# Optimization experiments

Measured on AMD Instinct MI355X. Metric: run time of the kernel, lower is better.

## Reference

```python
import jax, jax.numpy as jnp
import numpy as np

B, C, H, W = 16, 128, 128, 128
HEADS, DH = 4, 32          # hidden_dim = 128
GROUPS = 32                # min(dim // 4, 32)
EPS = 1e-5                 # eqx GroupNorm default


def setup_inputs() -> dict:
    key = jax.random.key(0)
    ks = jax.random.split(key, 8)
    hid = HEADS * DH
    return {
        "x": jax.random.normal(ks[0], (B, C, H, W), jnp.float32),
        "cond": jax.random.normal(ks[1], (B, C, H, W), jnp.float32),
        "gn_scale": jnp.ones((C,), jnp.float32),
        "gn_bias": jnp.zeros((C,), jnp.float32),
        "kv_w": jax.random.normal(ks[2], (2 * hid, C), jnp.float32) * 0.05,
        "kv_b": jax.random.normal(ks[3], (2 * hid,), jnp.float32) * 0.05,
        "q_w": jax.random.normal(ks[4], (hid, C), jnp.float32) * 0.05,
        "q_b": jax.random.normal(ks[5], (hid,), jnp.float32) * 0.05,
        "out_w": jax.random.normal(ks[6], (C, hid), jnp.float32) * 0.05,
        "out_b": jax.random.normal(ks[7], (C,), jnp.float32) * 0.05,
    }


def reference(x, cond, gn_scale, gn_bias, kv_w, kv_b, q_w, q_b, out_w, out_b):
    b, c, h, w = x.shape
    n = h * w
    # --- GroupNorm(32, dim) on x ---
    xg = x.reshape(b, GROUPS, c // GROUPS, h, w)
    mu = xg.mean(axis=(2, 3, 4), keepdims=True)
    var = xg.var(axis=(2, 3, 4), keepdims=True)
    xn = ((xg - mu) * jax.lax.rsqrt(var + EPS)).reshape(b, c, h, w)
    xn = xn * gn_scale[None, :, None, None] + gn_bias[None, :, None, None]
    # --- 1x1 conv projections (channel matmuls) ---
    kv = jnp.einsum('oc,bchw->bohw', kv_w, xn) + kv_b[None, :, None, None]
    q = jnp.einsum('oc,bchw->bohw', q_w, cond) + q_b[None, :, None, None]
    # split: channel layout is (kv, heads, dh)
    kv = kv.reshape(b, 2, HEADS, DH, n)
    k, v = kv[:, 0], kv[:, 1]          # [b, heads, dh, n]
    q = q.reshape(b, HEADS, DH, n)
    # --- linear-time attention: softmax over spatial positions ---
    k = jax.nn.softmax(k, axis=-1)
    context = jnp.einsum('bhdn,bhen->bhde', k, v)   # [b, heads, dh, dh]
    out = jnp.einsum('bhde,bhdn->bhen', context, q)  # [b, heads, dh, n]
    out = out.reshape(b, HEADS * DH, h, w)
    return jnp.einsum('oc,bchw->bohw', out_w, out) + out_b[None, :, None, None]
```

## Files before the change

### kernel.cpp

```cpp
#include <hip/hip_runtime.h>
#include <hip/hip_bf16.h>
#include <cstddef>

#define BATCH 16
#define CC 128
#define NN 16384
#define GROUPS 32
#define EPSV 1e-5f

#define OFF_MU    0
#define OFF_RSTD  512
#define OFF_BEFF  1024
#define OFF_CTX   5120
#define OFF_CB    70656
#define OFF_WH    334848
#define OFF_AH    596992
#define OFF_AL    728064
#define OFF_PART  859136
#define OFF_XT    5184512
#define PART_STRIDE 4224

typedef __attribute__((ext_vector_type(8))) short bf8;
typedef __attribute__((ext_vector_type(4))) float f4;
#define MFMA16(a,b,c) __builtin_amdgcn_mfma_f32_16x16x32_bf16(a,b,c,0,0,0)

__device__ inline unsigned short bf16_rtn(float f) {
    unsigned u = __builtin_bit_cast(unsigned, f);
    unsigned r = (u + 0x7FFFu + ((u >> 16) & 1u)) >> 16;
    return (unsigned short)r;
}
__device__ inline float bf16_f(unsigned short h) {
    unsigned u = ((unsigned)h) << 16;
    return __builtin_bit_cast(float, u);
}
__device__ inline unsigned cvtpk_bf16(float a, float b) {
    unsigned r;
    asm("v_cvt_pk_bf16_f32 %0, %1, %2" : "=v"(r) : "v"(a), "v"(b));
    return r;
}

__global__ __launch_bounds__(256) void k1a_fused(const float* __restrict__ src,
        unsigned short* __restrict__ xt, float* __restrict__ gp) {
    int b = blockIdx.y; int p0 = blockIdx.x * 128; int t = threadIdx.x;
    __shared__ unsigned short lh[128 * 136];
    int p = t & 127, chalf = t >> 7;
    const float* sp = src + (size_t)b * CC * NN + p0 + p;
    #pragma unroll 8
    for (int i = 0; i < 64; ++i) {
        int c = i * 2 + chalf;
        float v = sp[(size_t)c * NN];
        lh[p * 136 + c] = bf16_rtn(v);
    }
    __syncthreads();
    {
        int g = t >> 3, i8 = t & 7;
        float s = 0.f, sq = 0.f;
        for (int pp = i8 * 16; pp < i8 * 16 + 16; ++pp) {
            #pragma unroll
            for (int cc = 0; cc < 4; ++cc) {
                float v = bf16_f(lh[pp * 136 + g * 4 + cc]);
                s += v; sq += v * v;
            }
        }
        __shared__ float rs[256], rq[256];
        rs[t] = s; rq[t] = sq;
        __syncthreads();
        if (t < 32) {
            float a = 0.f, bq = 0.f;
            #pragma unroll
            for (int k = 0; k < 8; ++k) { a += rs[t * 8 + k]; bq += rq[t * 8 + k]; }
            float* d = gp + ((size_t)(b * 128 + blockIdx.x) * 32 + t) * 2;
            d[0] = a; d[1] = bq;
        }
    }
    int pr = t >> 4, c8 = (t & 15) * 8;
    #pragma unroll
    for (int j = 0; j < 8; ++j) {
        int p2 = j * 16 + pr;
        bf8 vh = *(const bf8*)&lh[p2 * 136 + c8];
        *(bf8*)&xt[((size_t)b * NN + p0 + p2) * 128 + c8] = vh;
    }
}

__global__ void k1b_stats(const float* __restrict__ gp, float* __restrict__ wsf) {
    int b = blockIdx.x; int t = threadIdx.x;
    int g = t & 31, sl = t >> 5;
    float s = 0.f, sq = 0.f;
    for (int j = sl; j < 128; j += 8) {
        const float* p = gp + ((size_t)(b * 128 + j) * 32 + g) * 2;
        s += p[0]; sq += p[1];
    }
    __shared__ float rs[256], rq[256];
    rs[t] = s; rq[t] = sq; __syncthreads();
    if (t < 32) {
        #pragma unroll
        for (int k = 1; k < 8; ++k) { s += rs[t + 32 * k]; sq += rq[t + 32 * k]; }
        float mean = s * (1.f / 65536.f);
        float var  = sq * (1.f / 65536.f) - mean * mean;
        wsf[OFF_MU + b * 32 + t]   = mean;
        wsf[OFF_RSTD + b * 32 + t] = rsqrtf(var + EPSV);
    }
}

__global__ __launch_bounds__(256) void k2_weff(const float* __restrict__ kv_w,
                        const float* __restrict__ kv_b,
                        const float* __restrict__ gn_scale, const float* __restrict__ gn_bias,
                        float* __restrict__ wsf, unsigned short* __restrict__ wh) {
    int b = blockIdx.y;
    int o0 = blockIdx.x * 32;
    int t = threadIdx.x;
    __shared__ float wrow[32 * 128];
    __shared__ float scl[128], sbm[128];
    __shared__ float bred[32][8];
    {
        const float4* src = (const float4*)(kv_w + (size_t)o0 * 128);
        float4* dst = (float4*)wrow;
        #pragma unroll
        for (int i = 0; i < 4; ++i) dst[i * 256 + t] = src[i * 256 + t];
        if (t < 128) {
            int g = t >> 2;
            float r = wsf[OFF_RSTD + b * 32 + g];
            float m = wsf[OFF_MU + b * 32 + g];
            float sc = gn_scale[t] * r;
            scl[t] = sc;
            sbm[t] = gn_bias[t] - m * sc;
        }
    }
    __syncthreads();
    int ol = t >> 3;
    int o  = o0 + ol;
    int q  = t & 7;
    {
        float bacc = 0.f;
        const float* wr = &wrow[ol * 128 + q * 16];
        #pragma unroll
        for (int c = 0; c < 16; ++c) bacc += wr[c] * sbm[q * 16 + c];
        bred[ol][q] = bacc;
    }
    int h  = (o & 127) >> 5;
    int ct = ((o >> 4) & 1) + ((o >= 128) ? 2 : 0);
    #pragma unroll
    for (int f2 = 0; f2 < 2; ++f2) {
        int f = 2 * q + f2;
        int ks = f >> 2, eq = f & 3;
        int c0 = ks * 32 + eq * 8;
        bf8 pk;
        #pragma unroll
        for (int e = 0; e < 8; ++e)
            pk[e] = (short)bf16_rtn(wrow[ol * 128 + c0 + e] * scl[c0 + e]);
        int lane = (o & 15) + 16 * eq;
        size_t fo = ((((size_t)b * 4 + h) * 4 + ct) * 4 + ks) * 512 + (size_t)lane * 8;
        *(bf8*)&wh[fo] = pk;
    }
    __syncthreads();
    if (q == 0) {
        float bacc = 0.f;
        #pragma unroll
        for (int k = 0; k < 8; ++k) bacc += bred[ol][k];
        wsf[OFF_BEFF + b * 256 + o] = kv_b[o] + bacc;
    }
}

__global__ __launch_bounds__(256) void k3_attn(
    const unsigned short* __restrict__ xt,
    const unsigned short* __restrict__ wh, const float* __restrict__ wsf,
    float* __restrict__ part)
{
    int b = blockIdx.y, chunk = blockIdx.x;
    int t = threadIdx.x, h = t >> 6, l = t & 63;
    int l15 = l & 15, lq = l >> 4;

    __shared__ unsigned short lds[4][2][32 * 64];

    bf8 W[4][4];
    #pragma unroll
    for (int ct = 0; ct < 4; ++ct)
      #pragma unroll
      for (int ks = 0; ks < 4; ++ks)
        W[ct][ks] = ((const bf8*)wh)[((((size_t)b*4 + h)*4 + ct)*4 + ks)*64 + l];

    float bk[4];
    #pragma unroll
    for (int ct = 0; ct < 4; ++ct) {
        int o = (ct < 2) ? (32*h + 16*ct + l15) : (128 + 32*h + 16*(ct-2) + l15);
        bk[ct] = wsf[OFF_BEFF + b * 256 + o];
    }

    bf8 ones;
    #pragma unroll
    for (int j = 0; j < 8; ++j) ones[j] = (short)0x3F80;

    f4 ctx[2][2]; f4 zac[2];
    #pragma unroll
    for (int i = 0; i < 2; ++i) {
        zac[i] = (f4){0,0,0,0};
        #pragma unroll
        for (int j = 0; j < 2; ++j) ctx[i][j] = (f4){0,0,0,0};
    }

    int pbase = chunk * 256;
    const unsigned short* xbase = xt + ((size_t)b * NN + pbase + l15) * 128 + lq * 8;
    #define FRAG(fp, ks) (*(const bf8*)(xbase + (size_t)(fp) * 2048 + (ks) * 32))

    bf8 pre[2][4];
    #pragma unroll
    for (int i = 0; i < 2; ++i)
      #pragma unroll
      for (int ks = 0; ks < 4; ++ks) pre[i][ks] = FRAG(i, ks);

    for (int tile = 0; tile < 4; ++tile) {
        #pragma unroll
        for (int half = 0; half < 2; ++half) {
            int nfp = tile * 4 + half * 2 + 2;
            int cfp = (nfp < 16) ? nfp : 0;
            bf8 nxt[2][4];
            #pragma unroll
            for (int i = 0; i < 2; ++i)
              #pragma unroll
              for (int ks = 0; ks < 4; ++ks) nxt[i][ks] = FRAG(cfp + i, ks);
            #pragma unroll
            for (int i = 0; i < 2; ++i) {
                int pt = half * 2 + i;
                f4 a4[4];
                #pragma unroll
                for (int ct = 0; ct < 4; ++ct) a4[ct] = (f4){0,0,0,0};
                #pragma unroll
                for (int ks = 0; ks < 4; ++ks) {
                    #pragma unroll
                    for (int ct = 0; ct < 4; ++ct)
                        a4[ct] = MFMA16(pre[i][ks], W[ct][ks], a4[ct]);
                }
                int p = pt * 16 + lq * 4;
                #pragma unroll
                for (int ct = 0; ct < 4; ++ct) {
                    int row = (ct & 1) * 16 + l15;
                    int sel = ct >> 1;
                    float v0 = a4[ct][0] + bk[ct];
                    float v1 = a4[ct][1] + bk[ct];
                    float v2 = a4[ct][2] + bk[ct];
                    float v3 = a4[ct][3] + bk[ct];
                    if (sel == 0) {
                        v0 = __expf(v0); v1 = __expf(v1);
                        v2 = __expf(v2); v3 = __expf(v3);
                    }
                    unsigned lo32 = cvtpk_bf16(v0, v1);
                    unsigned hi32 = cvtpk_bf16(v2, v3);
                    unsigned byte = ((unsigned)(row * 128 + p * 2)) ^ (((unsigned)(row & 7)) << 4);
                    *(uint2*)((char*)&lds[h][sel][0] + byte) = make_uint2(lo32, hi32);
                }
            }
            #pragma unroll
            for (int i = 0; i < 2; ++i)
              #pragma unroll
              for (int ks = 0; ks < 4; ++ks) pre[i][ks] = nxt[i][ks];
        }
        #pragma unroll
        for (int ks2 = 0; ks2 < 2; ++ks2) {
            int p8 = ks2 * 32 + lq * 8;
            bf8 ek[2], vv[2];
            #pragma unroll
            for (int dt = 0; dt < 2; ++dt) {
                int row = dt * 16 + l15;
                unsigned byte = ((unsigned)(row * 128 + p8 * 2)) ^ (((unsigned)(row & 7)) << 4);
                ek[dt] = *(const bf8*)((char*)&lds[h][0][0] + byte);
                vv[dt] = *(const bf8*)((char*)&lds[h][1][0] + byte);
            }
            #pragma unroll
            for (int dt = 0; dt < 2; ++dt) {
                #pragma unroll
                for (int et = 0; et < 2; ++et)
                    ctx[dt][et] = MFMA16(ek[dt], vv[et], ctx[dt][et]);
                zac[dt] = MFMA16(ek[dt], ones, zac[dt]);
            }
        }
    }
    #undef FRAG
    float* pb = part + (size_t)(b * 64 + chunk) * PART_STRIDE;
    #pragma unroll
    for (int dt = 0; dt < 2; ++dt) {
        #pragma unroll
        for (int et = 0; et < 2; ++et)
            #pragma unroll
            for (int j = 0; j < 4; ++j) {
                int d = 32*h + dt*16 + lq*4 + j;
                int e = et*16 + l15;
                pb[d * 32 + e] = ctx[dt][et][j];
            }
        if (l15 == 0)
            #pragma unroll
            for (int j = 0; j < 4; ++j)
                pb[4096 + 32*h + dt*16 + lq*4 + j] = zac[dt][j];
    }
}

__global__ __launch_bounds__(256) void k4_reduce(const float* __restrict__ part,
                                                 float* __restrict__ wsf, int nbpb) {
    int q = blockIdx.x, b = blockIdx.y;
    int tid = threadIdx.x;
    int hdl = tid >> 3;
    int hd = q * 32 + hdl;
    int e0 = (tid & 7) * 4;
    float s[4] = {0.f, 0.f, 0.f, 0.f};
    float z = 0.f;
    for (int i = 0; i < nbpb; ++i) {
        const float* pb = part + (size_t)(b * nbpb + i) * PART_STRIDE;
        float4 v = *(const float4*)&pb[hd * 32 + e0];
        s[0] += v.x; s[1] += v.y; s[2] += v.z; s[3] += v.w;
        if ((tid & 7) == 0) z += pb[4096 + hd];
    }
    __shared__ float zs[32];
    if ((tid & 7) == 0) zs[hdl] = z;
    __syncthreads();
    float zi = 1.f / zs[hdl];
    float* cg = wsf + OFF_CTX + (size_t)b * 4096;
    #pragma unroll
    for (int j = 0; j < 4; ++j) cg[hd * 32 + e0 + j] = s[j] * zi;
}

__global__ __launch_bounds__(256) void k5_buildA(const float* __restrict__ out_w,
                          const float* __restrict__ q_w,
                          const float* __restrict__ q_b, const float* __restrict__ out_b,
                          float* __restrict__ wsf,
                          unsigned short* __restrict__ ahp, unsigned short* __restrict__ alp) {
    int b = blockIdx.y;
    int oh = blockIdx.x * 16;
    int tid = threadIdx.x;
    __shared__ float ctx_p[128 * 33];
    __shared__ float T_s[16 * 132];
    {
        const float* src = wsf + OFF_CTX + (size_t)b * 4096;
        for (int i = tid; i < 4096; i += 256)
            ctx_p[(i >> 5) * 33 + (i & 31)] = src[i];
    }
    __syncthreads();
    int ol = tid >> 4;
    int o = oh + ol;
    int jb = tid & 15;
    int j0 = jb * 8;
    int h = j0 >> 5;
    {
        float ow[32];
        #pragma unroll
        for (int e4 = 0; e4 < 8; ++e4) {
            float4 v = *(const float4*)&out_w[o * 128 + h * 32 + e4 * 4];
            ow[e4*4+0]=v.x; ow[e4*4+1]=v.y; ow[e4*4+2]=v.z; ow[e4*4+3]=v.w;
        }
        #pragma unroll
        for (int dd = 0; dd < 8; ++dd) {
            int r = h * 32 + (j0 & 31) + dd;
            const float* cp = &ctx_p[r * 33];
            float a0 = 0.f, a1 = 0.f, a2 = 0.f, a3 = 0.f;
            #pragma unroll
            for (int e = 0; e < 32; e += 4) {
                a0 += ow[e+0] * cp[e+0];
                a1 += ow[e+1] * cp[e+1];
                a2 += ow[e+2] * cp[e+2];
                a3 += ow[e+3] * cp[e+3];
            }
            T_s[ol * 132 + j0 + dd] = (a0 + a1) + (a2 + a3);
        }
    }
    __syncthreads();
    {
        int ci0 = jb * 8;
        float a[8];
        #pragma unroll
        for (int i = 0; i < 8; ++i) a[i] = 0.f;
        for (int j = 0; j < 128; ++j) {
            float tv = T_s[ol * 132 + j];
            float4 v0 = *(const float4*)&q_w[j * 128 + ci0];
            float4 v1 = *(const float4*)&q_w[j * 128 + ci0 + 4];
            a[0] += tv*v0.x; a[1] += tv*v0.y; a[2] += tv*v0.z; a[3] += tv*v0.w;
            a[4] += tv*v1.x; a[5] += tv*v1.y; a[6] += tv*v1.z; a[7] += tv*v1.w;
        }
        int ks = ci0 >> 5;
        int eq = (ci0 >> 3) & 3;
        int lane = (o & 15) + 16 * eq;
        bf8 ph, pl;
        #pragma unroll
        for (int e = 0; e < 8; ++e) {
            unsigned short hh = bf16_rtn(a[e]);
            ph[e] = (short)hh;
            pl[e] = (short)bf16_rtn(a[e] - bf16_f(hh));
        }
        size_t fo = ((((size_t)b * 8 + (o >> 4)) * 4 + ks) * 64 + lane) * 8;
        *(bf8*)&ahp[fo] = ph;
        *(bf8*)&alp[fo] = pl;
        if (jb == 0) {
            float cb = 0.f;
            for (int j = 0; j < 128; ++j) cb += T_s[ol * 132 + j] * q_b[j];
            wsf[OFF_CB + b * 128 + o] = cb + out_b[o];
        }
    }
}

__global__ __launch_bounds__(256) void k6_mfma(
    const float* __restrict__ cond,
    const unsigned short* __restrict__ ahp, const unsigned short* __restrict__ alp,
    const float* __restrict__ wsf, float* __restrict__ y)
{
    int b = blockIdx.y, chunk = blockIdx.x;
    int t = threadIdx.x, w = t >> 6, l = t & 63, l15 = l & 15, lq = l >> 4;

    __shared__ __align__(16) unsigned short bfr[4][4][2][512];

    bf8 Ah[2][4], Al[2][4];
    #pragma unroll
    for (int r = 0; r < 2; ++r)
      #pragma unroll
      for (int ks = 0; ks < 4; ++ks) {
        size_t idx = (((size_t)b * 8 + (2*w + r)) * 4 + ks) * 64 + l;
        Ah[r][ks] = ((const bf8*)ahp)[idx];
        Al[r][ks] = ((const bf8*)alp)[idx];
      }
    float cbl[2][4];
    #pragma unroll
    for (int r = 0; r < 2; ++r)
      #pragma unroll
      for (int j = 0; j < 4; ++j)
        cbl[r][j] = wsf[OFF_CB + b*128 + (2*w + r)*16 + lq*4 + j];

    int pbase = chunk * 256;
    const float* cb0 = cond + (size_t)b * 128 * NN + pbase + w*16 + l15;

    float v[4][8];
    #pragma unroll
    for (int ks = 0; ks < 4; ++ks)
      #pragma unroll
      for (int j = 0; j < 8; ++j)
        v[ks][j] = cb0[(size_t)(ks*32 + lq*8 + j) * NN];

    for (int tile = 0; tile < 4; ++tile) {
        if (tile > 0) __syncthreads();
        #pragma unroll
        for (int ks = 0; ks < 4; ++ks) {
            union { unsigned u[4]; bf8 s; } uh, ul;
            #pragma unroll
            for (int q = 0; q < 4; ++q) {
                unsigned hp = cvtpk_bf16(v[ks][2*q], v[ks][2*q+1]);
                uh.u[q] = hp;
                float f0 = __builtin_bit_cast(float, hp << 16);
                float f1 = __builtin_bit_cast(float, hp & 0xFFFF0000u);
                ul.u[q] = cvtpk_bf16(v[ks][2*q] - f0, v[ks][2*q+1] - f1);
            }
            *(bf8*)&bfr[w][ks][0][l * 8] = uh.s;
            *(bf8*)&bfr[w][ks][1][l * 8] = ul.s;
        }
        __syncthreads();
        if (tile < 3) {
            const float* cp = cb0 + (tile + 1) * 64;
            #pragma unroll
            for (int ks = 0; ks < 4; ++ks)
              #pragma unroll
              for (int j = 0; j < 8; ++j)
                v[ks][j] = cp[(size_t)(ks*32 + lq*8 + j) * NN];
        }
        int tp = pbase + tile * 64;
        f4 acc[2][4];
        #pragma unroll
        for (int r = 0; r < 2; ++r)
          #pragma unroll
          for (int pt = 0; pt < 4; ++pt) acc[r][pt] = (f4){0,0,0,0};
        #pragma unroll
        for (int pt = 0; pt < 4; ++pt) {
            #pragma unroll
            for (int ks = 0; ks < 4; ++ks) {
                bf8 bh = *(const bf8*)&bfr[pt][ks][0][l * 8];
                bf8 bl = *(const bf8*)&bfr[pt][ks][1][l * 8];
                #pragma unroll
                for (int r = 0; r < 2; ++r) {
                    acc[r][pt] = MFMA16(Ah[r][ks], bh, acc[r][pt]);
                    acc[r][pt] = MFMA16(Al[r][ks], bh, acc[r][pt]);
                    acc[r][pt] = MFMA16(Ah[r][ks], bl, acc[r][pt]);
                }
            }
        }
        #pragma unroll
        for (int r = 0; r < 2; ++r)
          #pragma unroll
          for (int pt = 0; pt < 4; ++pt)
            #pragma unroll
            for (int j = 0; j < 4; ++j) {
                int o = (2*w + r)*16 + lq*4 + j;
                int p = tp + pt*16 + l15;
                y[((size_t)b*128 + o)*NN + p] = acc[r][pt][j] + cbl[r][j];
            }
    }
}

extern "C" void kernel_launch(void* const* d_in, const int* in_sizes, int n_in,
                              void* d_out, int out_size, void* d_ws, size_t ws_size,
                              hipStream_t stream) {
    const float* x        = (const float*)d_in[0];
    const float* cond     = (const float*)d_in[1];
    const float* gn_scale = (const float*)d_in[2];
    const float* gn_bias  = (const float*)d_in[3];
    const float* kv_w     = (const float*)d_in[4];
    const float* kv_b     = (const float*)d_in[5];
    const float* q_w      = (const float*)d_in[6];
    const float* q_b      = (const float*)d_in[7];
    const float* out_w    = (const float*)d_in[8];
    const float* out_b    = (const float*)d_in[9];
    float* y   = (float*)d_out;
    float* wsf = (float*)d_ws;

    unsigned short* WH = (unsigned short*)(wsf + OFF_WH);
    unsigned short* AH = (unsigned short*)(wsf + OFF_AH);
    unsigned short* AL = (unsigned short*)(wsf + OFF_AL);
    float* part = wsf + OFF_PART;

    bool big = ws_size >= (size_t)(OFF_XT + 16777216) * sizeof(float);

    unsigned short* XT;
    if (big) {
        XT = (unsigned short*)(wsf + OFF_XT);
    } else {
        XT = (unsigned short*)y;
    }

    k1a_fused<<<dim3(128, BATCH), 256, 0, stream>>>(x, XT, part);
    k1b_stats<<<BATCH, 256, 0, stream>>>(part, wsf);
    k2_weff<<<dim3(8, BATCH), 256, 0, stream>>>(kv_w, kv_b, gn_scale, gn_bias, wsf, WH);
    k3_attn<<<dim3(64, BATCH), 256, 0, stream>>>(XT, WH, wsf, part);
    k4_reduce<<<dim3(4, BATCH), 256, 0, stream>>>(part, wsf, 64);
    k5_buildA<<<dim3(8, BATCH), 256, 0, stream>>>(out_w, q_w, q_b, out_b, wsf, AH, AL);
    k6_mfma<<<dim3(64, BATCH), 256, 0, stream>>>(cond, AH, AL, wsf, y);
}
```

Before: 192.4 us.

## Fuse group-stats with weight folding and context reduce with A-matrix build

Merges the GroupNorm stats kernel into the effective-weight kernel, with one block per batch where each thread builds one output row of the folded kv weights. It also merges the partial-context reduction into the A-build kernel, so each block reduces the full 128x32 context into LDS and then processes two 16-row output slices. Two kernel launches and their global round-trips are removed. In exchange there is much less parallelism (16 blocks for the weight folding, each thread holding a 128-float register array) and the context reduction is repeated redundantly by 4 blocks per batch.

```diff
diff --git a/kernel.cpp b/kernel.cpp
--- a/kernel.cpp
+++ b/kernel.cpp
@@ -8,10 +8,7 @@
 #define GROUPS 32
 #define EPSV 1e-5f
 
-#define OFF_MU    0
-#define OFF_RSTD  512
 #define OFF_BEFF  1024
-#define OFF_CTX   5120
 #define OFF_CB    70656
 #define OFF_WH    334848
 #define OFF_AH    596992
@@ -82,83 +79,56 @@
     }
 }
 
-__global__ void k1b_stats(const float* __restrict__ gp, float* __restrict__ wsf) {
+__global__ void k12_weff(const float* __restrict__ gp,
+                         const float* __restrict__ kv_w, const float* __restrict__ kv_b,
+                         const float* __restrict__ gn_scale, const float* __restrict__ gn_bias,
+                         float* __restrict__ wsf, unsigned short* __restrict__ wh) {
     int b = blockIdx.x; int t = threadIdx.x;
-    int g = t & 31, sl = t >> 5;
-    float s = 0.f, sq = 0.f;
-    for (int j = sl; j < 128; j += 8) {
-        const float* p = gp + ((size_t)(b * 128 + j) * 32 + g) * 2;
-        s += p[0]; sq += p[1];
-    }
-    __shared__ float rs[256], rq[256];
-    rs[t] = s; rq[t] = sq; __syncthreads();
-    if (t < 32) {
-        #pragma unroll
-        for (int k = 1; k < 8; ++k) { s += rs[t + 32 * k]; sq += rq[t + 32 * k]; }
-        float mean = s * (1.f / 65536.f);
-        float var  = sq * (1.f / 65536.f) - mean * mean;
-        wsf[OFF_MU + b * 32 + t]   = mean;
-        wsf[OFF_RSTD + b * 32 + t] = rsqrtf(var + EPSV);
-    }
-}
-
-__global__ __launch_bounds__(256) void k2_weff(const float* __restrict__ kv_w,
-                        const float* __restrict__ kv_b,
-                        const float* __restrict__ gn_scale, const float* __restrict__ gn_bias,
-                        float* __restrict__ wsf, unsigned short* __restrict__ wh) {
-    int b = blockIdx.y;
-    int o0 = blockIdx.x * 32;
-    int t = threadIdx.x;
-    __shared__ float wrow[32 * 128];
-    __shared__ float scl[128], sbm[128];
-    __shared__ float bred[32][8];
+    __shared__ float mu_s[32], rs_s[32];
     {
-        const float4* src = (const float4*)(kv_w + (size_t)o0 * 128);
-        float4* dst = (float4*)wrow;
-        #pragma unroll
-        for (int i = 0; i < 4; ++i) dst[i * 256 + t] = src[i * 256 + t];
-        if (t < 128) {
-            int g = t >> 2;
-            float r = wsf[OFF_RSTD + b * 32 + g];
-            float m = wsf[OFF_MU + b * 32 + g];
-            float sc = gn_scale[t] * r;
-            scl[t] = sc;
-            sbm[t] = gn_bias[t] - m * sc;
-        }
-    }
-    __syncthreads();
-    int ol = t >> 3;
-    int o  = o0 + ol;
-    int q  = t & 7;
-    {
-        float bacc = 0.f;
-        const float* wr = &wrow[ol * 128 + q * 16];
-        #pragma unroll
-        for (int c = 0; c < 16; ++c) bacc += wr[c] * sbm[q * 16 + c];
-        bred[ol][q] = bacc;
-    }
+        int g = t & 31, sl = t >> 5;
+        float s = 0.f, sq = 0.f;
+        for (int j = sl; j < 128; j += 8) {
+            const float* p = gp + ((size_t)(b * 128 + j) * 32 + g) * 2;
+            s += p[0]; sq += p[1];
+        }
+        __shared__ float rs[256], rq[256];
+        rs[t] = s; rq[t] = sq; __syncthreads();
+        if (t < 32) {
+            #pragma unroll
+            for (int k = 1; k < 8; ++k) { s += rs[t + 32 * k]; sq += rq[t + 32 * k]; }
+            float mean = s * (1.f / 65536.f);
+            float var  = sq * (1.f / 65536.f) - mean * mean;
+            mu_s[t] = mean;
+            rs_s[t] = rsqrtf(var + EPSV);
+        }
+        __syncthreads();
+    }
+    int o = t;
+    float w[128]; float bacc = 0.f;
+    #pragma unroll
+    for (int c = 0; c < 128; ++c) {
+        int g = c >> 2;
+        float sc = gn_scale[c] * rs_s[g];
+        float kw = kv_w[o * 128 + c];
+        w[c] = kw * sc;
+        bacc += kw * (gn_bias[c] - mu_s[g] * sc);
+    }
+    wsf[OFF_BEFF + b * 256 + o] = kv_b[o] + bacc;
     int h  = (o & 127) >> 5;
     int ct = ((o >> 4) & 1) + ((o >= 128) ? 2 : 0);
-    #pragma unroll
-    for (int f2 = 0; f2 < 2; ++f2) {
-        int f = 2 * q + f2;
-        int ks = f >> 2, eq = f & 3;
-        int c0 = ks * 32 + eq * 8;
+    int i  = o & 15;
+    #pragma unroll
+    for (int ks = 0; ks < 4; ++ks)
+      #pragma unroll
+      for (int eq = 0; eq < 4; ++eq) {
         bf8 pk;
         #pragma unroll
-        for (int e = 0; e < 8; ++e)
-            pk[e] = (short)bf16_rtn(wrow[ol * 128 + c0 + e] * scl[c0 + e]);
-        int lane = (o & 15) + 16 * eq;
+        for (int e = 0; e < 8; ++e) pk[e] = (short)bf16_rtn(w[ks*32 + eq*8 + e]);
+        int lane = i + 16 * eq;
         size_t fo = ((((size_t)b * 4 + h) * 4 + ct) * 4 + ks) * 512 + (size_t)lane * 8;
         *(bf8*)&wh[fo] = pk;
-    }
-    __syncthreads();
-    if (q == 0) {
-        float bacc = 0.f;
-        #pragma unroll
-        for (int k = 0; k < 8; ++k) bacc += bred[ol][k];
-        wsf[OFF_BEFF + b * 256 + o] = kv_b[o] + bacc;
-    }
+      }
 }
 
 __global__ __launch_bounds__(256) void k3_attn(
@@ -293,104 +263,100 @@
     }
 }
 
-__global__ __launch_bounds__(256) void k4_reduce(const float* __restrict__ part,
-                                                 float* __restrict__ wsf, int nbpb) {
-    int q = blockIdx.x, b = blockIdx.y;
-    int tid = threadIdx.x;
-    int hdl = tid >> 3;
-    int hd = q * 32 + hdl;
-    int e0 = (tid & 7) * 4;
-    float s[4] = {0.f, 0.f, 0.f, 0.f};
-    float z = 0.f;
-    for (int i = 0; i < nbpb; ++i) {
-        const float* pb = part + (size_t)(b * nbpb + i) * PART_STRIDE;
-        float4 v = *(const float4*)&pb[hd * 32 + e0];
-        s[0] += v.x; s[1] += v.y; s[2] += v.z; s[3] += v.w;
-        if ((tid & 7) == 0) z += pb[4096 + hd];
-    }
-    __shared__ float zs[32];
-    if ((tid & 7) == 0) zs[hdl] = z;
-    __syncthreads();
-    float zi = 1.f / zs[hdl];
-    float* cg = wsf + OFF_CTX + (size_t)b * 4096;
-    #pragma unroll
-    for (int j = 0; j < 4; ++j) cg[hd * 32 + e0 + j] = s[j] * zi;
-}
-
-__global__ __launch_bounds__(256) void k5_buildA(const float* __restrict__ out_w,
-                          const float* __restrict__ q_w,
+__global__ __launch_bounds__(256) void k45_fused(const float* __restrict__ part,
+                          const float* __restrict__ out_w, const float* __restrict__ q_w,
                           const float* __restrict__ q_b, const float* __restrict__ out_b,
                           float* __restrict__ wsf,
                           unsigned short* __restrict__ ahp, unsigned short* __restrict__ alp) {
     int b = blockIdx.y;
-    int oh = blockIdx.x * 16;
     int tid = threadIdx.x;
     __shared__ float ctx_p[128 * 33];
     __shared__ float T_s[16 * 132];
+    __shared__ float zs[128];
     {
-        const float* src = wsf + OFF_CTX + (size_t)b * 4096;
-        for (int i = tid; i < 4096; i += 256)
-            ctx_p[(i >> 5) * 33 + (i & 31)] = src[i];
+        int hd = tid >> 1, e0 = (tid & 1) * 16;
+        float s[16];
+        #pragma unroll
+        for (int j = 0; j < 16; ++j) s[j] = 0.f;
+        float z = 0.f;
+        for (int i = 0; i < 64; ++i) {
+            const float* pb = part + (size_t)(b * 64 + i) * PART_STRIDE;
+            #pragma unroll
+            for (int j4 = 0; j4 < 4; ++j4) {
+                float4 v = *(const float4*)&pb[hd * 32 + e0 + j4 * 4];
+                s[j4*4+0] += v.x; s[j4*4+1] += v.y; s[j4*4+2] += v.z; s[j4*4+3] += v.w;
+            }
+            if ((tid & 1) == 0) z += pb[4096 + hd];
+        }
+        if ((tid & 1) == 0) zs[hd] = z;
+        __syncthreads();
+        float zi = 1.f / zs[hd];
+        #pragma unroll
+        for (int j = 0; j < 16; ++j) ctx_p[hd * 33 + e0 + j] = s[j] * zi;
     }
     __syncthreads();
     int ol = tid >> 4;
-    int o = oh + ol;
     int jb = tid & 15;
     int j0 = jb * 8;
     int h = j0 >> 5;
-    {
-        float ow[32];
-        #pragma unroll
-        for (int e4 = 0; e4 < 8; ++e4) {
-            float4 v = *(const float4*)&out_w[o * 128 + h * 32 + e4 * 4];
-            ow[e4*4+0]=v.x; ow[e4*4+1]=v.y; ow[e4*4+2]=v.z; ow[e4*4+3]=v.w;
-        }
-        #pragma unroll
-        for (int dd = 0; dd < 8; ++dd) {
-            int r = h * 32 + (j0 & 31) + dd;
-            const float* cp = &ctx_p[r * 33];
-            float a0 = 0.f, a1 = 0.f, a2 = 0.f, a3 = 0.f;
-            #pragma unroll
-            for (int e = 0; e < 32; e += 4) {
-                a0 += ow[e+0] * cp[e+0];
-                a1 += ow[e+1] * cp[e+1];
-                a2 += ow[e+2] * cp[e+2];
-                a3 += ow[e+3] * cp[e+3];
-            }
-            T_s[ol * 132 + j0 + dd] = (a0 + a1) + (a2 + a3);
-        }
-    }
-    __syncthreads();
-    {
-        int ci0 = jb * 8;
-        float a[8];
-        #pragma unroll
-        for (int i = 0; i < 8; ++i) a[i] = 0.f;
-        for (int j = 0; j < 128; ++j) {
-            float tv = T_s[ol * 132 + j];
-            float4 v0 = *(const float4*)&q_w[j * 128 + ci0];
-            float4 v1 = *(const float4*)&q_w[j * 128 + ci0 + 4];
-            a[0] += tv*v0.x; a[1] += tv*v0.y; a[2] += tv*v0.z; a[3] += tv*v0.w;
-            a[4] += tv*v1.x; a[5] += tv*v1.y; a[6] += tv*v1.z; a[7] += tv*v1.w;
-        }
-        int ks = ci0 >> 5;
-        int eq = (ci0 >> 3) & 3;
-        int lane = (o & 15) + 16 * eq;
-        bf8 ph, pl;
-        #pragma unroll
-        for (int e = 0; e < 8; ++e) {
-            unsigned short hh = bf16_rtn(a[e]);
-            ph[e] = (short)hh;
-            pl[e] = (short)bf16_rtn(a[e] - bf16_f(hh));
-        }
-        size_t fo = ((((size_t)b * 8 + (o >> 4)) * 4 + ks) * 64 + lane) * 8;
-        *(bf8*)&ahp[fo] = ph;
-        *(bf8*)&alp[fo] = pl;
-        if (jb == 0) {
-            float cb = 0.f;
-            for (int j = 0; j < 128; ++j) cb += T_s[ol * 132 + j] * q_b[j];
-            wsf[OFF_CB + b * 128 + o] = cb + out_b[o];
-        }
+    for (int c2 = 0; c2 < 2; ++c2) {
+        int oh = blockIdx.x * 32 + c2 * 16;
+        int o = oh + ol;
+        {
+            float ow[32];
+            #pragma unroll
+            for (int e4 = 0; e4 < 8; ++e4) {
+                float4 v = *(const float4*)&out_w[o * 128 + h * 32 + e4 * 4];
+                ow[e4*4+0]=v.x; ow[e4*4+1]=v.y; ow[e4*4+2]=v.z; ow[e4*4+3]=v.w;
+            }
+            #pragma unroll
+            for (int dd = 0; dd < 8; ++dd) {
+                int r = h * 32 + (j0 & 31) + dd;
+                const float* cp = &ctx_p[r * 33];
+                float a0 = 0.f, a1 = 0.f, a2 = 0.f, a3 = 0.f;
+                #pragma unroll
+                for (int e = 0; e < 32; e += 4) {
+                    a0 += ow[e+0] * cp[e+0];
+                    a1 += ow[e+1] * cp[e+1];
+                    a2 += ow[e+2] * cp[e+2];
+                    a3 += ow[e+3] * cp[e+3];
+                }
+                T_s[ol * 132 + j0 + dd] = (a0 + a1) + (a2 + a3);
+            }
+        }
+        __syncthreads();
+        {
+            int ci0 = jb * 8;
+            float a[8];
+            #pragma unroll
+            for (int i = 0; i < 8; ++i) a[i] = 0.f;
+            for (int j = 0; j < 128; ++j) {
+                float tv = T_s[ol * 132 + j];
+                float4 v0 = *(const float4*)&q_w[j * 128 + ci0];
+                float4 v1 = *(const float4*)&q_w[j * 128 + ci0 + 4];
+                a[0] += tv*v0.x; a[1] += tv*v0.y; a[2] += tv*v0.z; a[3] += tv*v0.w;
+                a[4] += tv*v1.x; a[5] += tv*v1.y; a[6] += tv*v1.z; a[7] += tv*v1.w;
+            }
+            int ks = ci0 >> 5;
+            int eq = (ci0 >> 3) & 3;
+            int lane = (o & 15) + 16 * eq;
+            bf8 ph, pl;
+            #pragma unroll
+            for (int e = 0; e < 8; ++e) {
+                unsigned short hh = bf16_rtn(a[e]);
+                ph[e] = (short)hh;
+                pl[e] = (short)bf16_rtn(a[e] - bf16_f(hh));
+            }
+            size_t fo = ((((size_t)b * 8 + (o >> 4)) * 4 + ks) * 64 + lane) * 8;
+            *(bf8*)&ahp[fo] = ph;
+            *(bf8*)&alp[fo] = pl;
+            if (jb == 0) {
+                float cb = 0.f;
+                for (int j = 0; j < 128; ++j) cb += T_s[ol * 132 + j] * q_b[j];
+                wsf[OFF_CB + b * 128 + o] = cb + out_b[o];
+            }
+        }
+        __syncthreads();
     }
 }
 
@@ -519,10 +485,8 @@
     }
 
     k1a_fused<<<dim3(128, BATCH), 256, 0, stream>>>(x, XT, part);
-    k1b_stats<<<BATCH, 256, 0, stream>>>(part, wsf);
-    k2_weff<<<dim3(8, BATCH), 256, 0, stream>>>(kv_w, kv_b, gn_scale, gn_bias, wsf, WH);
+    k12_weff<<<BATCH, 256, 0, stream>>>(part, kv_w, kv_b, gn_scale, gn_bias, wsf, WH);
     k3_attn<<<dim3(64, BATCH), 256, 0, stream>>>(XT, WH, wsf, part);
-    k4_reduce<<<dim3(4, BATCH), 256, 0, stream>>>(part, wsf, 64);
-    k5_buildA<<<dim3(8, BATCH), 256, 0, stream>>>(out_w, q_w, q_b, out_b, wsf, AH, AL);
+    k45_fused<<<dim3(4, BATCH), 256, 0, stream>>>(part, out_w, q_w, q_b, out_b, wsf, AH, AL);
     k6_mfma<<<dim3(64, BATCH), 256, 0, stream>>>(cond, AH, AL, wsf, y);
 }
```

Result: slower. 214.7 us (+11.6%).
